# Kernel tuning notes

Hardware: AMD Instinct MI355X
Metric: run time of the kernel (lower is better)

## Reference

```python
import jax, jax.numpy as jnp
import numpy as np

DIM = 512
HEADS = 16
WS = 7  # window size (cube), N = WS**3 = 343
B_ = 128
N = WS ** 3
TABLE = (2 * WS - 1) ** 3  # 2197


def _relative_position_index():
    coords = np.stack(np.meshgrid(np.arange(WS), np.arange(WS), np.arange(WS), indexing='ij'))  # [3,WS,WS,WS]
    cf = coords.reshape(3, -1)  # [3, N]
    rel = cf[:, :, None] - cf[:, None, :]  # [3, N, N]
    rel = rel.transpose(1, 2, 0).copy()
    rel[:, :, 0] += WS - 1
    rel[:, :, 1] += WS - 1
    rel[:, :, 2] += WS - 1
    rel[:, :, 0] *= (2 * WS - 1) * (2 * WS - 1)
    rel[:, :, 1] *= 2 * WS - 1
    return jnp.asarray(rel.sum(-1), dtype=jnp.int32)  # [N, N]


def setup_inputs() -> dict:
    key = jax.random.key(0)
    ks = jax.random.split(key, 8)
    x = jax.random.normal(ks[0], (B_, N, DIM), dtype=jnp.float32)
    q_global = jax.random.normal(ks[1], (1, DIM), dtype=jnp.float32)
    qkv_w = jax.random.normal(ks[2], (3 * DIM, DIM), dtype=jnp.float32) * (DIM ** -0.5)
    qkv_b = jax.random.normal(ks[3], (3 * DIM,), dtype=jnp.float32) * 0.02
    proj_w = jax.random.normal(ks[4], (DIM, DIM), dtype=jnp.float32) * (DIM ** -0.5)
    proj_b = jax.random.normal(ks[5], (DIM,), dtype=jnp.float32) * 0.02
    rel_bias_table = jax.random.normal(ks[6], (TABLE, HEADS), dtype=jnp.float32) * 0.02
    rel_pos_index = _relative_position_index()
    return {"x": x, "q_global": q_global, "qkv_w": qkv_w, "qkv_b": qkv_b,
            "rel_bias_table": rel_bias_table, "proj_w": proj_w, "proj_b": proj_b,
            "rel_pos_index": rel_pos_index}


def reference(x, q_global, qkv_w, qkv_b, rel_bias_table, proj_w, proj_b, rel_pos_index):
    B, Nt, C = x.shape
    hd = C // HEADS
    scale = hd ** -0.5
    # QKV projection (torch Linear: x @ W.T + b)
    qkv = (x @ qkv_w.T + qkv_b).reshape(B, Nt, 3, HEADS, hd)
    qkv = jnp.transpose(qkv, (2, 0, 3, 1, 4))  # [3, B, H, N, hd]
    q, k, v = qkv[0] * scale, qkv[1], qkv[2]
    attn = jnp.einsum('bhqd,bhkd->bhqk', q, k)  # [B, H, N, N]
    # relative position bias gather: table[idx] -> [N, N, H] -> [H, N, N]
    bias = rel_bias_table[rel_pos_index.reshape(-1)].reshape(Nt, Nt, HEADS)
    attn = attn + jnp.transpose(bias, (2, 0, 1))[None]
    attn = jax.nn.softmax(attn, axis=-1)
    out = jnp.einsum('bhqk,bhkd->bhqd', attn, v)  # [B, H, N, hd]
    out = jnp.transpose(out, (0, 2, 1, 3)).reshape(B, Nt, C)
    return out @ proj_w.T + proj_b
```

## Files before the change

kernel.cpp:

```cpp
#include <hip/hip_runtime.h>

typedef unsigned short u16;
typedef __attribute__((ext_vector_type(8))) short short8;
typedef __attribute__((ext_vector_type(4))) float f32x4;
typedef __attribute__((ext_vector_type(4))) unsigned uint4v;

#define NTOK 343
#define DIMC 512
#define HEADS_ 16
#define BATCH 128
#define MROWS 43904
#define TBL 117649

#define LOG2E 1.4426950408889634f
#define QSCALE (0.17677669529663687f * LOG2E)

__device__ __forceinline__ u16 f2bf(float f) {
  unsigned u = __builtin_bit_cast(unsigned, f);
  unsigned r = (u + 0x7fffu + ((u >> 16) & 1u)) >> 16;
  return (u16)r;
}
__device__ __forceinline__ float bf2f(u16 x) {
  return __builtin_bit_cast(float, ((unsigned)x) << 16);
}
__device__ __forceinline__ unsigned cvtpk(float lo, float hi) {
  unsigned r;
  asm("v_cvt_pk_bf16_f32 %0, %1, %2" : "=v"(r) : "v"(lo), "v"(hi));
  return r;
}

__global__ void cvt_f32_bf16_k(const float* __restrict__ in, u16* __restrict__ out, int n4) {
  int i = blockIdx.x * blockDim.x + threadIdx.x;
  int st = gridDim.x * blockDim.x;
  for (; i < n4; i += st) {
    float4 v = reinterpret_cast<const float4*>(in)[i];
    ushort4 o;
    o.x = f2bf(v.x); o.y = f2bf(v.y); o.z = f2bf(v.z); o.w = f2bf(v.w);
    reinterpret_cast<ushort4*>(out)[i] = o;
  }
}

__global__ void bias_pre_k(const float* __restrict__ table, const int* __restrict__ idx,
                           u16* __restrict__ biasB) {
  int t = blockIdx.x * 256 + threadIdx.x;
  if (t >= HEADS_ * 22 * 22 * 64) return;
  int l = t & 63;
  int tq = (t >> 6) % 22;
  int nt = ((t >> 6) / 22) % 22;
  int h = (t >> 6) / 484;
  int q = tq * 16 + (l & 15);
  int k0 = nt * 16 + (l >> 4) * 4;
  ushort4 o;
  u16* oe = (u16*)&o;
#pragma unroll
  for (int r = 0; r < 4; ++r) {
    int k = k0 + r;
    float v = (q < NTOK && k < NTOK) ? (LOG2E * table[idx[q * NTOK + k] * HEADS_ + h]) : -1e30f;
    oe[r] = f2bf(v);
  }
  *reinterpret_cast<ushort4*>(biasB + (size_t)t * 4) = o;
}

#define GLD16(gptr, lptr)                                                        \
  __builtin_amdgcn_global_load_lds(                                              \
      (const __attribute__((address_space(1))) void*)(const void*)(gptr),        \
      (__attribute__((address_space(3))) void*)(void*)(lptr), 16, 0, 0)

template <int EPI>
__global__ __launch_bounds__(256) void gemm_bt_k(const u16* __restrict__ A,
                                                 const u16* __restrict__ B,
                                                 const float* __restrict__ bias,
                                                 void* __restrict__ C, int N, int K) {
  const int NBL = N >> 7;
  int nwg = gridDim.x;
  int orig = blockIdx.x;
  int qq = nwg >> 3, rr = nwg & 7;
  int xcd = orig & 7, lid = orig >> 3;
  int bid = (xcd < rr ? xcd * (qq + 1) : rr * (qq + 1) + (xcd - rr) * qq) + lid;
  int mb = bid / NBL, nb = bid % NBL;
  __shared__ __align__(16) u16 As[2][128 * 64];
  __shared__ __align__(16) u16 Bs[2][128 * 64];
  int tid = threadIdx.x;
  int w = tid >> 6, l = tid & 63;
  int wr = w >> 1, wc = w & 1;
  f32x4 acc[4][4];
#pragma unroll
  for (int i = 0; i < 4; i++)
#pragma unroll
    for (int j = 0; j < 4; j++) acc[i][j] = (f32x4){0.f, 0.f, 0.f, 0.f};

  const int l8r = l >> 3, l8c = l & 7;
  const int woff = (w * 32) * 64;

#define STG2(kt, slot)                                                                    \
  {                                                                                       \
    _Pragma("unroll") for (int i4 = 0; i4 < 4; ++i4) {                                    \
      int rowl = w * 32 + i4 * 8 + l8r;                                                   \
      int cbs = (l8c * 16) ^ (((rowl >> 1) & 7) << 4);     \
      GLD16(A + (size_t)(mb * 128 + rowl) * K + (kt)*64 + (cbs >> 1),                     \
            As[slot] + woff + i4 * 512 + l * 8);                                          \
      GLD16(B + (size_t)(nb * 128 + rowl) * K + (kt)*64 + (cbs >> 1),                     \
            Bs[slot] + woff + i4 * 512 + l * 8);                                          \
    }                                                                                     \
  }

  int KT = K >> 6;
  STG2(0, 0);
  __syncthreads();
  for (int kt = 0; kt < KT; ++kt) {
    int cur = kt & 1;
    if (kt + 1 < KT) STG2(kt + 1, cur ^ 1);
#pragma unroll
    for (int kk = 0; kk < 2; ++kk) {
      short8 af[4], bf[4];
#pragma unroll
      for (int i = 0; i < 4; i++) {
        int off = (wr * 64 + i * 16 + (l & 15)) * 128 + kk * 64 + (l >> 4) * 16;
        off ^= ((off >> 8) & 7) << 4;
        af[i] = *reinterpret_cast<const short8*>((const u16*)As[cur] + (off >> 1));
      }
#pragma unroll
      for (int j = 0; j < 4; j++) {
        int off = (wc * 64 + j * 16 + (l & 15)) * 128 + kk * 64 + (l >> 4) * 16;
        off ^= ((off >> 8) & 7) << 4;
        bf[j] = *reinterpret_cast<const short8*>((const u16*)Bs[cur] + (off >> 1));
      }
#pragma unroll
      for (int i = 0; i < 4; i++)
#pragma unroll
        for (int j = 0; j < 4; j++)
          acc[i][j] = __builtin_amdgcn_mfma_f32_16x16x32_bf16(af[i], bf[j], acc[i][j], 0, 0, 0);
    }
    __syncthreads();
  }
#undef STG2

  int r0 = mb * 128 + wr * 64 + (l >> 4) * 4;
  int c0 = nb * 128 + wc * 64 + (l & 15);
#pragma unroll
  for (int j = 0; j < 4; j++) {
    int col = c0 + j * 16;
    float bv = bias[col];
    float mul = (EPI == 0 && col < 512) ? QSCALE : 1.0f;
#pragma unroll
    for (int i = 0; i < 4; i++) {
      int row = r0 + i * 16;
      if (EPI == 0) {
        u16* Cp = (u16*)C + (size_t)row * N + col;
#pragma unroll
        for (int r = 0; r < 4; r += 2) {
          unsigned pk = cvtpk((acc[i][j][r] + bv) * mul, (acc[i][j][r + 1] + bv) * mul);
          Cp[(size_t)r * N] = (u16)pk;
          Cp[(size_t)(r + 1) * N] = (u16)(pk >> 16);
        }
      } else {
#pragma unroll
        for (int r = 0; r < 4; r++)
          ((float*)C)[(size_t)(row + r) * N + col] = acc[i][j][r] + bv;
      }
    }
  }
}

__global__ __launch_bounds__(256, 3) void attn_k(const u16* __restrict__ qkv,
                                                 const u16* __restrict__ biasB,
                                                 u16* __restrict__ outA) {
  int p = blockIdx.x;
  int jj = p >> 3;
  int h = 2 * (p & 7) + (jj >> 7);
  int b = jj & 127;
  __shared__ __align__(16) u16 kS[352 * 40];
  __shared__ __align__(16) u16 vT[32 * 370];
  int tid = threadIdx.x;

  for (int idx = tid; idx < 352 * 4; idx += 256) {
    int row = idx >> 2, seg = idx & 3;
    uint4 vk = {0, 0, 0, 0};
    if (row < NTOK)
      vk = *reinterpret_cast<const uint4*>(qkv + (size_t)(b * NTOK + row) * 1536 + 512 +
                                           h * 32 + seg * 8);
    *reinterpret_cast<uint4*>(kS + row * 40 + seg * 8) = vk;
  }
  for (int idx = tid; idx < NTOK * 4; idx += 256) {
    int row = idx >> 2, seg = idx & 3;
    size_t base = (size_t)(b * NTOK + row) * 1536 + 1024 + h * 32 + seg * 8;
    uint4 vv = *reinterpret_cast<const uint4*>(qkv + base);
    const u16* e = reinterpret_cast<const u16*>(&vv);
#pragma unroll
    for (int t = 0; t < 8; ++t) vT[(seg * 8 + t) * 370 + row] = e[t];
  }
  for (int idx = tid; idx < 32 * 9; idx += 256) vT[(idx / 9) * 370 + NTOK + (idx % 9)] = 0;
  __syncthreads();

  int w = tid >> 6, l = tid & 63;
  const int cl = l & 15, q4 = l >> 4;
  const f32x4 z4 = (f32x4){0.f, 0.f, 0.f, 0.f};
  for (int tq = w; tq < 22; tq += 4) {
    short8 bq = (short8){0, 0, 0, 0, 0, 0, 0, 0};
    int qrow = tq * 16 + cl;
    if (qrow < NTOK)
      bq = *reinterpret_cast<const short8*>(qkv + (size_t)(b * NTOK + qrow) * 1536 + h * 32 +
                                            q4 * 8);
    unsigned pk[22][2];
    float tot = 0.f;
    const u16* bbase = biasB + ((size_t)(h * 22) * 22 + tq) * 256 + l * 4;
#pragma unroll
    for (int nt = 0; nt < 22; ++nt) {
      short8 ak = *reinterpret_cast<const short8*>(kS + (nt * 16 + cl) * 40 + q4 * 8);
      f32x4 s = __builtin_amdgcn_mfma_f32_16x16x32_bf16(ak, bq, z4, 0, 0, 0);
      ushort4 bb = *reinterpret_cast<const ushort4*>(bbase + (size_t)nt * 22 * 256);
      const u16* be = (const u16*)&bb;
      float e0 = __builtin_amdgcn_exp2f(s[0] + bf2f(be[0]));
      float e1 = __builtin_amdgcn_exp2f(s[1] + bf2f(be[1]));
      float e2 = __builtin_amdgcn_exp2f(s[2] + bf2f(be[2]));
      float e3 = __builtin_amdgcn_exp2f(s[3] + bf2f(be[3]));
      tot += (e0 + e1) + (e2 + e3);
      pk[nt][0] = cvtpk(e0, e1);
      pk[nt][1] = cvtpk(e2, e3);
    }
    tot += __builtin_bit_cast(float, __shfl_xor(__builtin_bit_cast(int, tot), 16));
    tot += __builtin_bit_cast(float, __shfl_xor(__builtin_bit_cast(int, tot), 32));
    float inv = 1.0f / tot;
    float ir[4];
#pragma unroll
    for (int r = 0; r < 4; ++r)
      ir[r] = __shfl(inv, q4 * 4 + r);

    f32x4 O0 = z4, O1 = z4;
#pragma unroll
    for (int kt = 0; kt < 11; ++kt) {
      unsigned v16_0 = (q4 & 2) ? pk[2 * kt + 1][0] : pk[2 * kt][0];
      unsigned v16_1 = (q4 & 2) ? pk[2 * kt + 1][1] : pk[2 * kt][1];
      unsigned v32_0 = (q4 & 2) ? pk[2 * kt][0] : pk[2 * kt + 1][0];
      unsigned v32_1 = (q4 & 2) ? pk[2 * kt][1] : pk[2 * kt + 1][1];
      unsigned t1_0 = (unsigned)__shfl_xor((int)v16_0, 16);
      unsigned t1_1 = (unsigned)__shfl_xor((int)v16_1, 16);
      unsigned t2_0 = (unsigned)__shfl_xor((int)v32_0, 32);
      unsigned t2_1 = (unsigned)__shfl_xor((int)v32_1, 32);
      unsigned t3_0 = (unsigned)__shfl_xor((int)t2_0, 16);
      unsigned t3_1 = (unsigned)__shfl_xor((int)t2_1, 16);
      unsigned f0 = (q4 & 1) ? ((q4 & 2) ? t1_0 : t3_0) : ((q4 & 2) ? t2_0 : v16_0);
      unsigned f1 = (q4 & 1) ? ((q4 & 2) ? t1_1 : t3_1) : ((q4 & 2) ? t2_1 : v16_1);
      unsigned s0 = (q4 & 1) ? ((q4 & 2) ? v16_0 : t2_0) : ((q4 & 2) ? t3_0 : t1_0);
      unsigned s1 = (q4 & 1) ? ((q4 & 2) ? v16_1 : t2_1) : ((q4 & 2) ? t3_1 : t1_1);
      uint4v ap = (uint4v){f0, f1, s0, s1};
      short8 bv0 = *reinterpret_cast<const short8*>(vT + cl * 370 + kt * 32 + q4 * 8);
      short8 bv1 = *reinterpret_cast<const short8*>(vT + (16 + cl) * 370 + kt * 32 + q4 * 8);
      O0 = __builtin_amdgcn_mfma_f32_16x16x32_bf16(__builtin_bit_cast(short8, ap), bv0, O0,
                                                   0, 0, 0);
      O1 = __builtin_amdgcn_mfma_f32_16x16x32_bf16(__builtin_bit_cast(short8, ap), bv1, O1,
                                                   0, 0, 0);
    }
#pragma unroll
    for (int r = 0; r < 4; ++r) {
      int qr2 = tq * 16 + q4 * 4 + r;
      if (qr2 < NTOK) {
        unsigned pko = cvtpk(O0[r] * ir[r], O1[r] * ir[r]);
        u16* op = outA + (size_t)(b * NTOK + qr2) * 512 + h * 32 + cl;
        op[0] = (u16)pko;
        op[16] = (u16)(pko >> 16);
      }
    }
  }
}

extern "C" void kernel_launch(void* const* d_in, const int* in_sizes, int n_in,
                              void* d_out, int out_size, void* d_ws, size_t ws_size,
                              hipStream_t stream) {
  const float* x      = (const float*)d_in[0];
  const float* qkv_w  = (const float*)d_in[2];
  const float* qkv_b  = (const float*)d_in[3];
  const float* table  = (const float*)d_in[4];
  const float* proj_w = (const float*)d_in[5];
  const float* proj_b = (const float*)d_in[6];
  const int*   relidx = (const int*)d_in[7];

  char* ws = (char*)d_ws;
  u16*   x_bf  = (u16*)(ws);
  u16*   qw_bf = (u16*)(ws + 44957696);
  u16*   pw_bf = (u16*)(ws + 46530560);
  u16*   qkv_o = (u16*)(ws + 47054848);
  u16*   biasB = (u16*)(ws + 181927936);

  cvt_f32_bf16_k<<<2048, 256, 0, stream>>>(x, x_bf, (BATCH * NTOK * DIMC) / 4);
  cvt_f32_bf16_k<<<768, 256, 0, stream>>>(qkv_w, qw_bf, (3 * DIMC * DIMC) / 4);
  cvt_f32_bf16_k<<<256, 256, 0, stream>>>(proj_w, pw_bf, (DIMC * DIMC) / 4);
  bias_pre_k<<<(HEADS_ * 22 * 22 * 64 + 255) / 256, 256, 0, stream>>>(table, relidx, biasB);

  gemm_bt_k<0><<<343 * 12, 256, 0, stream>>>(x_bf, qw_bf, qkv_b, qkv_o, 1536, 512);
  attn_k<<<BATCH * HEADS_, 256, 0, stream>>>(qkv_o, biasB, x_bf);
  gemm_bt_k<1><<<343 * 4, 256, 0, stream>>>(x_bf, pw_bf, proj_b, d_out, 512, 512);
}
```

Baseline: 280.5 us.

## Fuse fp32-to-bf16 conversion of x into QKV GEMM A-tile loading

Drops the standalone kernel that converted the whole fp32 input to bf16. The QKV GEMM now loads fp32 A tiles into registers, packs them to bf16 and writes them into the swizzled LDS buffer after the MFMA work of each k-step, keeping double buffering. This removes a full read-and-write pass over the activation tensor and one launch. In exchange the GEMM reads twice as many A bytes from global/L2 across its 12 column blocks, loses the direct global-to-LDS path for A, and holds more registers.

```diff
diff --git a/kernel.cpp b/kernel.cpp
--- a/kernel.cpp
+++ b/kernel.cpp
@@ -67,7 +67,7 @@
       (__attribute__((address_space(3))) void*)(void*)(lptr), 16, 0, 0)
 
 template <int EPI>
-__global__ __launch_bounds__(256) void gemm_bt_k(const u16* __restrict__ A,
+__global__ __launch_bounds__(256) void gemm_bt_k(const void* __restrict__ Av,
                                                  const u16* __restrict__ B,
                                                  const float* __restrict__ bias,
                                                  void* __restrict__ C, int N, int K) {
@@ -90,26 +90,62 @@
     for (int j = 0; j < 4; j++) acc[i][j] = (f32x4){0.f, 0.f, 0.f, 0.f};
 
   const int l8r = l >> 3, l8c = l & 7;
-  const int woff = (w * 32) * 64;
-
-#define STG2(kt, slot)                                                                    \
-  {                                                                                       \
-    _Pragma("unroll") for (int i4 = 0; i4 < 4; ++i4) {                                    \
-      int rowl = w * 32 + i4 * 8 + l8r;                                                   \
-      int cbs = (l8c * 16) ^ (((rowl >> 1) & 7) << 4);     \
-      GLD16(A + (size_t)(mb * 128 + rowl) * K + (kt)*64 + (cbs >> 1),                     \
-            As[slot] + woff + i4 * 512 + l * 8);                                          \
-      GLD16(B + (size_t)(nb * 128 + rowl) * K + (kt)*64 + (cbs >> 1),                     \
-            Bs[slot] + woff + i4 * 512 + l * 8);                                          \
-    }                                                                                     \
+
+  float4 fa[4][2];
+
+#define LDA_F32(kt)                                                                  \
+  {                                                                                  \
+    _Pragma("unroll") for (int i4 = 0; i4 < 4; ++i4) {                               \
+      int rw = w * 32 + i4 * 8 + l8r;                                                \
+      int ce = ((l8c * 16) ^ (((rw >> 1) & 7) << 4)) >> 1;                           \
+      const float* src = (const float*)Av + (size_t)(mb * 128 + rw) * K + (kt)*64 + ce; \
+      fa[i4][0] = *reinterpret_cast<const float4*>(src);                             \
+      fa[i4][1] = *reinterpret_cast<const float4*>(src + 4);                         \
+    }                                                                                \
+  }
+#define WRA_F32(slot)                                                                \
+  {                                                                                  \
+    _Pragma("unroll") for (int i4 = 0; i4 < 4; ++i4) {                               \
+      int rw = w * 32 + i4 * 8 + l8r;                                                \
+      uint4v wv;                                                                     \
+      wv.x = cvtpk(fa[i4][0].x, fa[i4][0].y);                                        \
+      wv.y = cvtpk(fa[i4][0].z, fa[i4][0].w);                                        \
+      wv.z = cvtpk(fa[i4][1].x, fa[i4][1].y);                                        \
+      wv.w = cvtpk(fa[i4][1].z, fa[i4][1].w);                                        \
+      *reinterpret_cast<uint4v*>(&As[slot][rw * 64 + l8c * 8]) = wv;                 \
+    }                                                                                \
+  }
+#define LDA_BF(kt, slot)                                                             \
+  {                                                                                  \
+    _Pragma("unroll") for (int i4 = 0; i4 < 4; ++i4) {                               \
+      int rw = w * 32 + i4 * 8 + l8r;                                                \
+      int cbs = (l8c * 16) ^ (((rw >> 1) & 7) << 4);                                 \
+      GLD16((const u16*)Av + (size_t)(mb * 128 + rw) * K + (kt)*64 + (cbs >> 1),     \
+            As[slot] + w * 32 * 64 + i4 * 512 + l * 8);                              \
+    }                                                                                \
+  }
+#define LDB_BF(kt, slot)                                                             \
+  {                                                                                  \
+    _Pragma("unroll") for (int i4 = 0; i4 < 4; ++i4) {                               \
+      int rw = w * 32 + i4 * 8 + l8r;                                                \
+      int cbs = (l8c * 16) ^ (((rw >> 1) & 7) << 4);                                 \
+      GLD16(B + (size_t)(nb * 128 + rw) * K + (kt)*64 + (cbs >> 1),                  \
+            Bs[slot] + w * 32 * 64 + i4 * 512 + l * 8);                              \
+    }                                                                                \
   }
 
   int KT = K >> 6;
-  STG2(0, 0);
+  if (EPI == 0) { LDA_F32(0); } else { LDA_BF(0, 0); }
+  LDB_BF(0, 0);
+  if (EPI == 0) { WRA_F32(0); }
   __syncthreads();
+
   for (int kt = 0; kt < KT; ++kt) {
     int cur = kt & 1;
-    if (kt + 1 < KT) STG2(kt + 1, cur ^ 1);
+    if (kt + 1 < KT) {
+      if (EPI == 0) { LDA_F32(kt + 1); } else { LDA_BF(kt + 1, cur ^ 1); }
+      LDB_BF(kt + 1, cur ^ 1);
+    }
 #pragma unroll
     for (int kk = 0; kk < 2; ++kk) {
       short8 af[4], bf[4];
@@ -131,9 +167,13 @@
         for (int j = 0; j < 4; j++)
           acc[i][j] = __builtin_amdgcn_mfma_f32_16x16x32_bf16(af[i], bf[j], acc[i][j], 0, 0, 0);
     }
+    if (EPI == 0 && kt + 1 < KT) { WRA_F32(cur ^ 1); }
     __syncthreads();
   }
-#undef STG2
+#undef LDA_F32
+#undef WRA_F32
+#undef LDA_BF
+#undef LDB_BF
 
   int r0 = mb * 128 + wr * 64 + (l >> 4) * 4;
   int c0 = nb * 128 + wc * 64 + (l & 15);
@@ -276,18 +316,17 @@
   const int*   relidx = (const int*)d_in[7];
 
   char* ws = (char*)d_ws;
-  u16*   x_bf  = (u16*)(ws);
+  u16*   attnO = (u16*)(ws);
   u16*   qw_bf = (u16*)(ws + 44957696);
   u16*   pw_bf = (u16*)(ws + 46530560);
   u16*   qkv_o = (u16*)(ws + 47054848);
   u16*   biasB = (u16*)(ws + 181927936);
 
-  cvt_f32_bf16_k<<<2048, 256, 0, stream>>>(x, x_bf, (BATCH * NTOK * DIMC) / 4);
   cvt_f32_bf16_k<<<768, 256, 0, stream>>>(qkv_w, qw_bf, (3 * DIMC * DIMC) / 4);
   cvt_f32_bf16_k<<<256, 256, 0, stream>>>(proj_w, pw_bf, (DIMC * DIMC) / 4);
   bias_pre_k<<<(HEADS_ * 22 * 22 * 64 + 255) / 256, 256, 0, stream>>>(table, relidx, biasB);
 
-  gemm_bt_k<0><<<343 * 12, 256, 0, stream>>>(x_bf, qw_bf, qkv_b, qkv_o, 1536, 512);
-  attn_k<<<BATCH * HEADS_, 256, 0, stream>>>(qkv_o, biasB, x_bf);
-  gemm_bt_k<1><<<343 * 4, 256, 0, stream>>>(x_bf, pw_bf, proj_b, d_out, 512, 512);
-}
+  gemm_bt_k<0><<<343 * 12, 256, 0, stream>>>(x, qw_bf, qkv_b, qkv_o, 1536, 512);
+  attn_k<<<BATCH * HEADS_, 256, 0, stream>>>(qkv_o, biasB, attnO);
+  gemm_bt_k<1><<<343 * 4, 256, 0, stream>>>(attnO, pw_bf, proj_b, d_out, 512, 512);
+}
```

New measurement: 315.4 us. 12.4% more time.

## Switch attention kernel to 32x32x16 MFMA tiles with fused online PV accumulation

Applied to the files above, without the earlier changes.

Rewrites the attention inner loop to use 32x32x16 bf16 MFMA tiles over 11 query/key tiles instead of 16x16x32 over 22. P·V is now accumulated inside the key loop rather than after storing all probabilities, which removes the 22-entry packed register array and simplifies the lane shuffles. The bias precompute layout is reordered to match the new accumulator layout. Tradeoffs: only 11 query tiles across 4 waves, so load is uneven, and the output is written with scalar 16-bit stores.

```diff
diff --git a/kernel.cpp b/kernel.cpp
--- a/kernel.cpp
+++ b/kernel.cpp
@@ -3,6 +3,7 @@
 typedef unsigned short u16;
 typedef __attribute__((ext_vector_type(8))) short short8;
 typedef __attribute__((ext_vector_type(4))) float f32x4;
+typedef __attribute__((ext_vector_type(16))) float f32x16;
 typedef __attribute__((ext_vector_type(4))) unsigned uint4v;
 
 #define NTOK 343
@@ -43,22 +44,27 @@
 __global__ void bias_pre_k(const float* __restrict__ table, const int* __restrict__ idx,
                            u16* __restrict__ biasB) {
   int t = blockIdx.x * 256 + threadIdx.x;
-  if (t >= HEADS_ * 22 * 22 * 64) return;
-  int l = t & 63;
-  int tq = (t >> 6) % 22;
-  int nt = ((t >> 6) / 22) % 22;
-  int h = (t >> 6) / 484;
-  int q = tq * 16 + (l & 15);
-  int k0 = nt * 16 + (l >> 4) * 4;
+  if (t >= HEADS_ * 121 * 256) return;
+  int r4 = t & 3;
+  int l = (t >> 2) & 63;
+  int rest = t >> 8;
+  int tq = rest % 11;
+  int nt = (rest / 11) % 11;
+  int h = rest / 121;
+  int q = tq * 32 + (l & 31);
+  int hi = l >> 5;
   ushort4 o;
   u16* oe = (u16*)&o;
 #pragma unroll
-  for (int r = 0; r < 4; ++r) {
-    int k = k0 + r;
-    float v = (q < NTOK && k < NTOK) ? (LOG2E * table[idx[q * NTOK + k] * HEADS_ + h]) : -1e30f;
-    oe[r] = f2bf(v);
-  }
-  *reinterpret_cast<ushort4*>(biasB + (size_t)t * 4) = o;
+  for (int rr = 0; rr < 4; ++rr) {
+    int r = r4 * 4 + rr;
+    int tok = nt * 32 + (r & 3) + 8 * (r >> 2) + 4 * hi;
+    float v = (q < NTOK && tok < NTOK) ? (LOG2E * table[idx[q * NTOK + tok] * HEADS_ + h])
+                                       : -1e30f;
+    oe[rr] = f2bf(v);
+  }
+  *reinterpret_cast<ushort4*>(biasB +
+                              (size_t)(((h * 11 + nt) * 11 + tq) * 1024 + l * 16 + r4 * 4)) = o;
 }
 
 #define GLD16(gptr, lptr)                                                        \
@@ -96,7 +102,7 @@
   {                                                                                       \
     _Pragma("unroll") for (int i4 = 0; i4 < 4; ++i4) {                                    \
       int rowl = w * 32 + i4 * 8 + l8r;                                                   \
-      int cbs = (l8c * 16) ^ (((rowl >> 1) & 7) << 4);     \
+      int cbs = (l8c * 16) ^ (((rowl >> 1) & 7) << 4);                                    \
       GLD16(A + (size_t)(mb * 128 + rowl) * K + (kt)*64 + (cbs >> 1),                     \
             As[slot] + woff + i4 * 512 + l * 8);                                          \
       GLD16(B + (size_t)(nb * 128 + rowl) * K + (kt)*64 + (cbs >> 1),                     \
@@ -193,72 +199,70 @@
   __syncthreads();
 
   int w = tid >> 6, l = tid & 63;
-  const int cl = l & 15, q4 = l >> 4;
-  const f32x4 z4 = (f32x4){0.f, 0.f, 0.f, 0.f};
-  for (int tq = w; tq < 22; tq += 4) {
-    short8 bq = (short8){0, 0, 0, 0, 0, 0, 0, 0};
-    int qrow = tq * 16 + cl;
-    if (qrow < NTOK)
-      bq = *reinterpret_cast<const short8*>(qkv + (size_t)(b * NTOK + qrow) * 1536 + h * 32 +
-                                            q4 * 8);
-    unsigned pk[22][2];
+  const int d32 = l & 31, hi = l >> 5;
+  const bool upHalf = (hi != 0);
+
+  for (int tq = w; tq < 11; tq += 4) {
+    int qrow = tq * 32 + d32;
+    short8 bq0 = (short8){0, 0, 0, 0, 0, 0, 0, 0};
+    short8 bq1 = (short8){0, 0, 0, 0, 0, 0, 0, 0};
+    if (qrow < NTOK) {
+      const u16* qb = qkv + (size_t)(b * NTOK + qrow) * 1536 + h * 32 + hi * 8;
+      bq0 = *reinterpret_cast<const short8*>(qb);
+      bq1 = *reinterpret_cast<const short8*>(qb + 16);
+    }
+    f32x16 O = {0, 0, 0, 0, 0, 0, 0, 0, 0, 0, 0, 0, 0, 0, 0, 0};
     float tot = 0.f;
-    const u16* bbase = biasB + ((size_t)(h * 22) * 22 + tq) * 256 + l * 4;
-#pragma unroll
-    for (int nt = 0; nt < 22; ++nt) {
-      short8 ak = *reinterpret_cast<const short8*>(kS + (nt * 16 + cl) * 40 + q4 * 8);
-      f32x4 s = __builtin_amdgcn_mfma_f32_16x16x32_bf16(ak, bq, z4, 0, 0, 0);
-      ushort4 bb = *reinterpret_cast<const ushort4*>(bbase + (size_t)nt * 22 * 256);
-      const u16* be = (const u16*)&bb;
-      float e0 = __builtin_amdgcn_exp2f(s[0] + bf2f(be[0]));
-      float e1 = __builtin_amdgcn_exp2f(s[1] + bf2f(be[1]));
-      float e2 = __builtin_amdgcn_exp2f(s[2] + bf2f(be[2]));
-      float e3 = __builtin_amdgcn_exp2f(s[3] + bf2f(be[3]));
-      tot += (e0 + e1) + (e2 + e3);
-      pk[nt][0] = cvtpk(e0, e1);
-      pk[nt][1] = cvtpk(e2, e3);
-    }
-    tot += __builtin_bit_cast(float, __shfl_xor(__builtin_bit_cast(int, tot), 16));
+    const u16* bbase = biasB + ((size_t)(h * 121 + tq)) * 1024 + l * 16;
+    for (int nt = 0; nt < 11; ++nt) {
+      const u16* kr = kS + (nt * 32 + d32) * 40 + hi * 8;
+      short8 ak0 = *reinterpret_cast<const short8*>(kr);
+      short8 ak1 = *reinterpret_cast<const short8*>(kr + 16);
+      f32x16 S = {0, 0, 0, 0, 0, 0, 0, 0, 0, 0, 0, 0, 0, 0, 0, 0};
+      S = __builtin_amdgcn_mfma_f32_32x32x16_bf16(ak0, bq0, S, 0, 0, 0);
+      S = __builtin_amdgcn_mfma_f32_32x32x16_bf16(ak1, bq1, S, 0, 0, 0);
+      const u16* bp = bbase + (size_t)nt * 11 * 1024;
+      short8 bb0 = *reinterpret_cast<const short8*>(bp);
+      short8 bb1 = *reinterpret_cast<const short8*>(bp + 8);
+      float ex[16];
+#pragma unroll
+      for (int r = 0; r < 16; ++r) {
+        u16 bw = (u16)((r < 8) ? bb0[r] : bb1[r - 8]);
+        float v = S[r] + bf2f(bw);
+        ex[r] = __builtin_amdgcn_exp2f(v);
+        tot += ex[r];
+      }
+      unsigned W[8];
+#pragma unroll
+      for (int r2 = 0; r2 < 8; ++r2) W[r2] = cvtpk(ex[2 * r2], ex[2 * r2 + 1]);
+#pragma unroll
+      for (int c = 0; c < 2; ++c) {
+        unsigned x0 = W[4 * c + 0], x1 = W[4 * c + 1];
+        unsigned y0 = W[4 * c + 2], y1 = W[4 * c + 3];
+        unsigned x0s = (unsigned)__shfl_xor((int)x0, 32);
+        unsigned x1s = (unsigned)__shfl_xor((int)x1, 32);
+        unsigned y0s = (unsigned)__shfl_xor((int)y0, 32);
+        unsigned y1s = (unsigned)__shfl_xor((int)y1, 32);
+        uint4v ap;
+        ap.x = upHalf ? y0s : x0;
+        ap.y = upHalf ? y1s : x1;
+        ap.z = upHalf ? y0 : x0s;
+        ap.w = upHalf ? y1 : x1s;
+        short8 bv = *reinterpret_cast<const short8*>(vT + d32 * 370 + nt * 32 + c * 16 + hi * 8);
+        O = __builtin_amdgcn_mfma_f32_32x32x16_bf16(__builtin_bit_cast(short8, ap), bv, O,
+                                                    0, 0, 0);
+      }
+    }
     tot += __builtin_bit_cast(float, __shfl_xor(__builtin_bit_cast(int, tot), 32));
     float inv = 1.0f / tot;
-    float ir[4];
-#pragma unroll
-    for (int r = 0; r < 4; ++r)
-      ir[r] = __shfl(inv, q4 * 4 + r);
-
-    f32x4 O0 = z4, O1 = z4;
-#pragma unroll
-    for (int kt = 0; kt < 11; ++kt) {
-      unsigned v16_0 = (q4 & 2) ? pk[2 * kt + 1][0] : pk[2 * kt][0];
-      unsigned v16_1 = (q4 & 2) ? pk[2 * kt + 1][1] : pk[2 * kt][1];
-      unsigned v32_0 = (q4 & 2) ? pk[2 * kt][0] : pk[2 * kt + 1][0];
-      unsigned v32_1 = (q4 & 2) ? pk[2 * kt][1] : pk[2 * kt + 1][1];
-      unsigned t1_0 = (unsigned)__shfl_xor((int)v16_0, 16);
-      unsigned t1_1 = (unsigned)__shfl_xor((int)v16_1, 16);
-      unsigned t2_0 = (unsigned)__shfl_xor((int)v32_0, 32);
-      unsigned t2_1 = (unsigned)__shfl_xor((int)v32_1, 32);
-      unsigned t3_0 = (unsigned)__shfl_xor((int)t2_0, 16);
-      unsigned t3_1 = (unsigned)__shfl_xor((int)t2_1, 16);
-      unsigned f0 = (q4 & 1) ? ((q4 & 2) ? t1_0 : t3_0) : ((q4 & 2) ? t2_0 : v16_0);
-      unsigned f1 = (q4 & 1) ? ((q4 & 2) ? t1_1 : t3_1) : ((q4 & 2) ? t2_1 : v16_1);
-      unsigned s0 = (q4 & 1) ? ((q4 & 2) ? v16_0 : t2_0) : ((q4 & 2) ? t3_0 : t1_0);
-      unsigned s1 = (q4 & 1) ? ((q4 & 2) ? v16_1 : t2_1) : ((q4 & 2) ? t3_1 : t1_1);
-      uint4v ap = (uint4v){f0, f1, s0, s1};
-      short8 bv0 = *reinterpret_cast<const short8*>(vT + cl * 370 + kt * 32 + q4 * 8);
-      short8 bv1 = *reinterpret_cast<const short8*>(vT + (16 + cl) * 370 + kt * 32 + q4 * 8);
-      O0 = __builtin_amdgcn_mfma_f32_16x16x32_bf16(__builtin_bit_cast(short8, ap), bv0, O0,
-                                                   0, 0, 0);
-      O1 = __builtin_amdgcn_mfma_f32_16x16x32_bf16(__builtin_bit_cast(short8, ap), bv1, O1,
-                                                   0, 0, 0);
-    }
-#pragma unroll
-    for (int r = 0; r < 4; ++r) {
-      int qr2 = tq * 16 + q4 * 4 + r;
-      if (qr2 < NTOK) {
-        unsigned pko = cvtpk(O0[r] * ir[r], O1[r] * ir[r]);
-        u16* op = outA + (size_t)(b * NTOK + qr2) * 512 + h * 32 + cl;
-        op[0] = (u16)pko;
-        op[16] = (u16)(pko >> 16);
+#pragma unroll
+    for (int r = 0; r < 16; ++r) {
+      int qloc = (r & 3) + 8 * (r >> 2) + 4 * hi;
+      float ir = __shfl(inv, qloc);
+      int q = tq * 32 + qloc;
+      if (q < NTOK) {
+        float ov = O[r] * ir;
+        outA[(size_t)(b * NTOK + q) * 512 + h * 32 + d32] = (u16)cvtpk(ov, ov);
       }
     }
   }
@@ -285,7 +289,7 @@
   cvt_f32_bf16_k<<<2048, 256, 0, stream>>>(x, x_bf, (BATCH * NTOK * DIMC) / 4);
   cvt_f32_bf16_k<<<768, 256, 0, stream>>>(qkv_w, qw_bf, (3 * DIMC * DIMC) / 4);
   cvt_f32_bf16_k<<<256, 256, 0, stream>>>(proj_w, pw_bf, (DIMC * DIMC) / 4);
-  bias_pre_k<<<(HEADS_ * 22 * 22 * 64 + 255) / 256, 256, 0, stream>>>(table, relidx, biasB);
+  bias_pre_k<<<1936, 256, 0, stream>>>(table, relidx, biasB);
 
   gemm_bt_k<0><<<343 * 12, 256, 0, stream>>>(x_bf, qw_bf, qkv_b, qkv_o, 1536, 512);
   attn_k<<<BATCH * HEADS_, 256, 0, stream>>>(qkv_o, biasB, x_bf);
```

Result: faster. 263.1 us (-6.2%).
